# Optimization experiments

Hardware: AMD Instinct MI355X
Metric: run time of the kernel (lower is better)

Reference implementation:

```python
import jax, jax.numpy as jnp
import numpy as np

L, B, D = 1024, 4, 1024
E, K, H = 8, 2, 4096


def setup_inputs() -> dict:
    key = jax.random.key(0)
    ks = jax.random.split(key, 12)
    s_g = 1.0 / np.sqrt(D)
    s_h = 1.0 / np.sqrt(H)
    return {
        "inputs": jax.random.normal(ks[0], (L, B, D), jnp.float32),
        "task_param": jax.random.normal(ks[1], (B, D), jnp.float32),
        "gate_img_w": jax.random.normal(ks[2], (D, E), jnp.float32) * s_g,
        "gate_img_b": jnp.zeros((E,), jnp.float32),
        "gate_txt_w": jax.random.normal(ks[3], (D, E), jnp.float32) * s_g,
        "gate_txt_b": jnp.zeros((E,), jnp.float32),
        "task_gate_w": jax.random.normal(ks[4], (D, E), jnp.float32) * s_g,
        "task_gate_b": jnp.zeros((E,), jnp.float32),
        "alpha": jnp.float32(0.5),
        "w1": jax.random.normal(ks[5], (E, D, H), jnp.float32) * s_g,
        "w2": jax.random.normal(ks[6], (E, H, D), jnp.float32) * s_h,
        "is_text": 1,
    }


def reference(inputs, task_param, gate_img_w, gate_img_b, gate_txt_w, gate_txt_b,
              task_gate_w, task_gate_b, alpha, w1, w2, is_text):
    # task gate: (B, E) -> broadcast over L
    task_logits = (task_param @ task_gate_w + task_gate_b)[None]  # (1, B, E)
    if is_text:
        input_logits = inputs @ gate_txt_w + gate_txt_b  # (L, B, E)
    else:
        input_logits = inputs @ gate_img_w + gate_img_b
    gate_logits = (1.0 - alpha) * input_logits + alpha * task_logits  # (L, B, E)

    topk_vals, sel = jax.lax.top_k(gate_logits, K)  # (L, B, K)

    # auxiliary load-balancing loss
    soft = jax.nn.softmax(gate_logits.astype(jnp.float32), axis=-1)
    avg_weight = soft.mean(axis=(0, 1))                       # (E,)
    expert_mask = jax.nn.one_hot(sel, E).sum(axis=2)          # (L, B, E)
    avg_count = expert_mask.mean(axis=(0, 1))                 # (E,)
    l_aux = jnp.mean(avg_weight * avg_count) * E

    # renormalized top-k weights, combined per expert: (L, B, E)
    weights = jax.nn.softmax(topk_vals.astype(jnp.float32), axis=-1).astype(inputs.dtype)
    comb = jnp.sum(jax.nn.one_hot(sel, E, dtype=weights.dtype) * weights[..., None], axis=2)

    # dense per-expert FFN, weighted combine (loop over fixed small E)
    results = jnp.zeros_like(inputs)
    for e in range(E):
        h = jax.nn.gelu(inputs @ w1[e])      # (L, B, H)
        out = h @ w2[e]                      # (L, B, D)
        results = results + comb[..., e:e + 1] * out
    return results, l_aux.astype(jnp.float32)
```

## Files before the change

kernel.cpp:

```cpp
#include <hip/hip_runtime.h>
#include <hip/hip_bf16.h>
#include <math.h>

#define L_ 1024
#define B_ 4
#define D_ 1024
#define E_ 8
#define K_ 2
#define H_ 4096
#define T_ (L_*B_)
#define P_ (T_*K_)
#define PPAD (P_+256)

typedef unsigned short u16;
typedef __attribute__((ext_vector_type(4))) float f32x4;
typedef __attribute__((ext_vector_type(8))) short s16x8;

__device__ __forceinline__ u16 f2bf(float f) {
  uint32_t u = __float_as_uint(f);
  uint32_t r = (u + 0x7FFFu + ((u >> 16) & 1u)) >> 16;
  return (u16)r;
}
__device__ __forceinline__ float bf2f(u16 v) {
  return __uint_as_float((uint32_t)v << 16);
}
__device__ __forceinline__ float gelu_fast(float v) {
  float u = v * (1.0f + 0.044715f * v * v);
  float t = __expf(-1.5957691216057308f * u);
  return v / (1.0f + t);
}


__device__ void conv_block(const float* __restrict__ src, u16* __restrict__ dst,
                           int R, int C, int r0, int c0) {
  __shared__ float tile[64][65];
  int t = threadIdx.x;
  int tr = t >> 4, tc = (t & 15) * 4;
#pragma unroll
  for (int p = 0; p < 4; ++p) {
    int r = tr + p * 16;
    float4 v = *(const float4*)(src + (size_t)(r0 + r) * C + c0 + tc);
    tile[r][tc] = v.x; tile[r][tc+1] = v.y; tile[r][tc+2] = v.z; tile[r][tc+3] = v.w;
  }
  __syncthreads();
#pragma unroll
  for (int p = 0; p < 4; ++p) {
    int c = tr + p * 16;
    ushort4 o;
    o.x = f2bf(tile[tc+0][c]); o.y = f2bf(tile[tc+1][c]);
    o.z = f2bf(tile[tc+2][c]); o.w = f2bf(tile[tc+3][c]);
    *(ushort4*)(dst + (size_t)(c0 + c) * R + r0 + tc) = o;
  }
}

__global__ void prep(const float* __restrict__ w1, u16* __restrict__ w1b,
                     const float* __restrict__ w2, u16* __restrict__ w2b,
                     const float* __restrict__ x, const float* __restrict__ task_param,
                     const float* __restrict__ gw_img, const float* __restrict__ gb_img,
                     const float* __restrict__ gw_txt, const float* __restrict__ gb_txt,
                     const float* __restrict__ tgw, const float* __restrict__ tgb,
                     const float* __restrict__ alpha_p, const int* __restrict__ is_text_p,
                     float4* __restrict__ sel_w, float* __restrict__ prob_part,
                     int* __restrict__ count_part) {
  int gid = blockIdx.x;
  if (gid < 8192) {
    int gx = gid & 63, gy = (gid >> 6) & 15, e = gid >> 10;
    conv_block(w1 + (size_t)e * D_ * H_, w1b + (size_t)e * D_ * H_,
               D_, H_, gy * 64, gx * 64);
    return;
  }
  if (gid < 16384) {
    int g = gid - 8192;
    int gx = g & 15, gy = (g >> 4) & 63, e = g >> 10;
    conv_block(w2 + (size_t)e * D_ * H_, w2b + (size_t)e * D_ * H_,
               H_, D_, gy * 64, gx * 64);
    return;
  }
  int bid = gid - 16384;
  __shared__ float wprob[4][8];
  __shared__ int wcnt[4][8];
  int wid = threadIdx.x >> 6, lane = threadIdx.x & 63;
  int t = bid * 4 + wid;
  int b = t & (B_ - 1);
  int it = is_text_p[0];
  const float* gw = it ? gw_txt : gw_img;
  const float* gb = it ? gb_txt : gb_img;
  float alpha = alpha_p[0];
  const float* xr = x + (size_t)t * D_;
  const float* tp = task_param + (size_t)b * D_;
  float acc[8] = {0,0,0,0,0,0,0,0};
  float tac[8] = {0,0,0,0,0,0,0,0};
  for (int i = 0; i < D_/64; ++i) {
    int d = i * 64 + lane;
    float xv = xr[d], tv = tp[d];
#pragma unroll
    for (int e = 0; e < 8; ++e) {
      acc[e] += xv * gw[d*8 + e];
      tac[e] += tv * tgw[d*8 + e];
    }
  }
#pragma unroll
  for (int e = 0; e < 8; ++e) {
#pragma unroll
    for (int off = 32; off > 0; off >>= 1) {
      acc[e] += __shfl_xor(acc[e], off);
      tac[e] += __shfl_xor(tac[e], off);
    }
  }
  float lg[8];
#pragma unroll
  for (int e = 0; e < 8; ++e)
    lg[e] = (1.0f - alpha) * (acc[e] + gb[e]) + alpha * (tac[e] + tgb[e]);
  float m = lg[0];
#pragma unroll
  for (int e = 1; e < 8; ++e) m = fmaxf(m, lg[e]);
  float pr[8], ps = 0.f;
#pragma unroll
  for (int e = 0; e < 8; ++e) { pr[e] = expf(lg[e] - m); ps += pr[e]; }
  float inv = 1.0f / ps;
  int i0 = 0; float v0 = lg[0];
#pragma unroll
  for (int e = 1; e < 8; ++e) if (lg[e] > v0) { v0 = lg[e]; i0 = e; }
  int i1 = -1; float v1 = -1e30f;
#pragma unroll
  for (int e = 0; e < 8; ++e) if (e != i0 && lg[e] > v1) { v1 = lg[e]; i1 = e; }
  float ex = expf(v1 - v0);
  float w0 = 1.0f / (1.0f + ex), w1v = ex / (1.0f + ex);
  if (lane == 0) {
    sel_w[t] = make_float4(__int_as_float(i0), __int_as_float(i1), w0, w1v);
#pragma unroll
    for (int e = 0; e < 8; ++e) {
      wprob[wid][e] = pr[e] * inv;
      wcnt[wid][e] = (i0 == e) + (i1 == e);
    }
  }
  __syncthreads();
  if (threadIdx.x < 8) {
    int e = threadIdx.x;
    prob_part[bid * 8 + e] = wprob[0][e] + wprob[1][e] + wprob[2][e] + wprob[3][e];
    count_part[bid * 8 + e] = wcnt[0][e] + wcnt[1][e] + wcnt[2][e] + wcnt[3][e];
  }
}

__global__ void finalize(const float* __restrict__ prob_part, const int* __restrict__ count_part,
                         int* __restrict__ meta, float* __restrict__ laux_out) {
  __shared__ float ps_[256];
  __shared__ int cs_[256];
  int t = threadIdx.x;
  int e = t & 7, s = t >> 3;
  float p = 0.f; int c = 0;
  for (int b = s; b < 1024; b += 32) { p += prob_part[b*8 + e]; c += count_part[b*8 + e]; }
  ps_[t] = p; cs_[t] = c;
  __syncthreads();
  for (int st = 16; st > 0; st >>= 1) {
    if (s < st) { ps_[t] += ps_[t + st*8]; cs_[t] += cs_[t + st*8]; }
    __syncthreads();
  }
  if (t == 0) {
    int off = 0; float laux = 0.f;
    int u1 = 0, u2 = 0;
    for (int ee = 0; ee < 8; ++ee) {
      int cnt = cs_[ee];
      meta[ee] = cnt;
      meta[8 + ee] = off;
      meta[16 + ee] = off;
      int nb = (cnt + 255) >> 8;
      meta[24 + ee] = nb;
      meta[32 + ee] = u1;
      meta[41 + ee] = u2;
      u1 += 16 * nb;
      u2 += 4 * nb * 2;
      off += cnt;
      laux += (ps_[ee] * (1.0f/4096.0f)) * ((float)cnt * (1.0f/4096.0f));
    }
    meta[32 + 8] = u1;
    meta[41 + 8] = u2;
    meta[50] = 0;
    meta[51] = 0;
    *laux_out = laux;
  }
}

__global__ void scatter_gather(const float* __restrict__ x, const float4* __restrict__ sel_w,
                               int* __restrict__ cursors, float* __restrict__ pair_w,
                               int* __restrict__ pair_idx, u16* __restrict__ Xg) {
  int wid = threadIdx.x >> 6, lane = threadIdx.x & 63;
  int t = blockIdx.x * 4 + wid;
  float4 sw = sel_w[t];
  int s0 = __float_as_int(sw.x), s1 = __float_as_int(sw.y);
  int p0 = 0, p1 = 0;
  if (lane == 0) {
    p0 = atomicAdd(&cursors[s0], 1);
    p1 = atomicAdd(&cursors[s1], 1);
  }
  p0 = __shfl(p0, 0); p1 = __shfl(p1, 0);
  if (lane == 0) {
    pair_w[p0] = sw.z; pair_w[p1] = sw.w;
    pair_idx[t*2] = p0; pair_idx[t*2+1] = p1;
  }
  const float* xr = x + (size_t)t * D_;
  u16* d0 = Xg + (size_t)p0 * D_;
  u16* d1 = Xg + (size_t)p1 * D_;
#pragma unroll
  for (int i = 0; i < 4; ++i) {
    int c = i * 256 + lane * 4;
    float4 v = *(const float4*)(xr + c);
    ushort4 o;
    o.x = f2bf(v.x); o.y = f2bf(v.y); o.z = f2bf(v.z); o.w = f2bf(v.w);
    *(ushort4*)(d0 + c) = o;
    *(ushort4*)(d1 + c) = o;
  }
}

template<int EPI, int KDIM, int KLEN, int NOUT, int NPANEL, int KSPLIT>
__global__ __launch_bounds__(512, 2)
void gemm256(const u16* __restrict__ Tok, const u16* __restrict__ Wt,
             int* __restrict__ meta, const float* __restrict__ pair_w,
             u16* __restrict__ Hout, u16* __restrict__ Cout) {
  const int* offs = meta + 8;
  const int* nbx  = meta + 24;
  const int* ub   = (EPI == 0) ? meta + 32 : meta + 41;
  int* tick       = meta + ((EPI == 0) ? 50 : 51);

  __shared__ u16 As[2][16384];
  __shared__ u16 Bs[2][16384];
  __shared__ int s_u;
  int t = threadIdx.x, lane = t & 63, wid = t >> 6;
  int wf = wid & 1, wt = wid >> 1;

  int goff[4]; int ldso[4];
#pragma unroll
  for (int i = 0; i < 4; ++i) {
    int slot = i * 512 + t;
    int row = slot >> 3;
    int kk = (slot & 7) ^ (row & 7);
    goff[i] = row * KDIM + kk * 8;
    ldso[i] = slot * 8;
  }

  int aoff[8][2], boff[4][2];
#pragma unroll
  for (int r = 0; r < 8; ++r) {
    int row = wf * 128 + r * 16 + (lane & 15);
#pragma unroll
    for (int h = 0; h < 2; ++h) {
      int kk = h * 4 + (lane >> 4);
      aoff[r][h] = (row * 8 + (kk ^ (row & 7))) * 8;
    }
  }
#pragma unroll
  for (int f = 0; f < 4; ++f) {
    int row = wt * 64 + f * 16 + (lane & 15);
#pragma unroll
    for (int h = 0; h < 2; ++h) {
      int kk = h * 4 + (lane >> 4);
      boff[f][h] = (row * 8 + (kk ^ (row & 7))) * 8;
    }
  }

  constexpr int NT = KLEN / 64;
  int lr = lane & 15, lg4 = (lane >> 4) * 4;
  int Utot = ub[8];

  for (;;) {
    if (t == 0) s_u = atomicAdd(tick, 1);
    __syncthreads();
    int u = s_u;
    if (u >= Utot) break;
    int e = 0;
    while (u >= ub[e + 1]) ++e;
    int ul = u - ub[e];
    int nb = nbx[e];
    int panel = ul / (nb * KSPLIT);
    int rem   = ul - panel * (nb * KSPLIT);
    int bx    = rem / KSPLIT;
    int ks    = rem - bx * KSPLIT;
    int ne  = meta[e];
    int off = offs[e];
    int kbase = ks * KLEN;
    u16* Cpart = Cout + (size_t)ks * P_ * D_;
    const u16* Wg = Wt + (size_t)e * NOUT * KDIM + (size_t)panel * 256 * KDIM + kbase;
    const u16* Tg = Tok + (size_t)(off + bx * 256) * KDIM + kbase;

    f32x4 acc[8][4] = {};
#pragma unroll
    for (int i = 0; i < 4; ++i) {
      __builtin_amdgcn_global_load_lds(
          (const __attribute__((address_space(1))) void*)(Wg + goff[i]),
          (__attribute__((address_space(3))) void*)(&As[0][ldso[i]]), 16, 0, 0);
      __builtin_amdgcn_global_load_lds(
          (const __attribute__((address_space(1))) void*)(Tg + goff[i]),
          (__attribute__((address_space(3))) void*)(&Bs[0][ldso[i]]), 16, 0, 0);
    }
    __syncthreads();
    int cur = 0;
    for (int tt = 0; tt < NT; ++tt) {
      if (tt + 1 < NT) {
        int k0 = (tt + 1) * 64;
        int nbuf = cur ^ 1;
#pragma unroll
        for (int i = 0; i < 4; ++i) {
          __builtin_amdgcn_global_load_lds(
              (const __attribute__((address_space(1))) void*)(Wg + goff[i] + k0),
              (__attribute__((address_space(3))) void*)(&As[nbuf][ldso[i]]), 16, 0, 0);
          __builtin_amdgcn_global_load_lds(
              (const __attribute__((address_space(1))) void*)(Tg + goff[i] + k0),
              (__attribute__((address_space(3))) void*)(&Bs[nbuf][ldso[i]]), 16, 0, 0);
        }
      }
      const u16* Ab = &As[cur][0]; const u16* Bb = &Bs[cur][0];
#pragma unroll
      for (int h = 0; h < 2; ++h) {
        s16x8 a[8], b[4];
#pragma unroll
        for (int r = 0; r < 8; ++r) a[r] = *(const s16x8*)(Ab + aoff[r][h]);
#pragma unroll
        for (int f = 0; f < 4; ++f) b[f] = *(const s16x8*)(Bb + boff[f][h]);
#pragma unroll
        for (int r = 0; r < 8; ++r)
#pragma unroll
          for (int f = 0; f < 4; ++f)
            acc[r][f] = __builtin_amdgcn_mfma_f32_16x16x32_bf16(a[r], b[f], acc[r][f], 0, 0, 0);
      }
      __syncthreads();
      cur ^= 1;
    }

#pragma unroll
    for (int f = 0; f < 4; ++f) {
      int tokl = bx * 256 + wt * 64 + f * 16 + lr;
      if (tokl >= ne) continue;
      size_t grow = (size_t)(off + tokl);
      if (EPI == 0) {
#pragma unroll
        for (int r = 0; r < 8; ++r) {
          ushort4 o;
          o.x = f2bf(gelu_fast(acc[r][f][0]));
          o.y = f2bf(gelu_fast(acc[r][f][1]));
          o.z = f2bf(gelu_fast(acc[r][f][2]));
          o.w = f2bf(gelu_fast(acc[r][f][3]));
          *(ushort4*)(Hout + grow * NOUT + panel * 256 + wf * 128 + r * 16 + lg4) = o;
        }
      } else {
        float w = pair_w[grow];
#pragma unroll
        for (int r = 0; r < 8; ++r) {
          ushort4 o;
          o.x = f2bf(acc[r][f][0] * w); o.y = f2bf(acc[r][f][1] * w);
          o.z = f2bf(acc[r][f][2] * w); o.w = f2bf(acc[r][f][3] * w);
          *(ushort4*)(Cpart + grow * NOUT + panel * 256 + wf * 128 + r * 16 + lg4) = o;
        }
      }
    }
  }
}

__global__ void combine(const u16* __restrict__ pair_out, const int* __restrict__ pair_idx,
                        float* __restrict__ out) {
  const u16* part1 = pair_out + (size_t)P_ * D_;
  int t = blockIdx.x;
  int p0 = pair_idx[t*2], p1 = pair_idx[t*2+1];
  int c = threadIdx.x * 4;
  ushort4 a0 = *(const ushort4*)(pair_out + (size_t)p0 * D_ + c);
  ushort4 a1 = *(const ushort4*)(part1    + (size_t)p0 * D_ + c);
  ushort4 b0 = *(const ushort4*)(pair_out + (size_t)p1 * D_ + c);
  ushort4 b1 = *(const ushort4*)(part1    + (size_t)p1 * D_ + c);
  float4 o;
  o.x = (bf2f(a0.x) + bf2f(a1.x)) + (bf2f(b0.x) + bf2f(b1.x));
  o.y = (bf2f(a0.y) + bf2f(a1.y)) + (bf2f(b0.y) + bf2f(b1.y));
  o.z = (bf2f(a0.z) + bf2f(a1.z)) + (bf2f(b0.z) + bf2f(b1.z));
  o.w = (bf2f(a0.w) + bf2f(a1.w)) + (bf2f(b0.w) + bf2f(b1.w));
  *(float4*)(out + (size_t)t * D_ + c) = o;
}

extern "C" void kernel_launch(void* const* d_in, const int* in_sizes, int n_in,
                              void* d_out, int out_size, void* d_ws, size_t ws_size,
                              hipStream_t stream) {
  const float* inputs      = (const float*)d_in[0];
  const float* task_param  = (const float*)d_in[1];
  const float* gate_img_w  = (const float*)d_in[2];
  const float* gate_img_b  = (const float*)d_in[3];
  const float* gate_txt_w  = (const float*)d_in[4];
  const float* gate_txt_b  = (const float*)d_in[5];
  const float* task_gate_w = (const float*)d_in[6];
  const float* task_gate_b = (const float*)d_in[7];
  const float* alpha       = (const float*)d_in[8];
  const float* w1          = (const float*)d_in[9];
  const float* w2          = (const float*)d_in[10];
  const int*   is_text     = (const int*)d_in[11];
  float* out = (float*)d_out;

  char* ws = (char*)d_ws;
  u16* w1b = (u16*)(ws + 0);
  u16* w2b = (u16*)(ws + 67108864);
  u16* Xg  = (u16*)(ws + 134217728);
  u16* Hb  = (u16*)(ws + 151519232);
  float4* sel_w   = (float4*)(ws + 220725248);
  float* pair_w   = (float*)(ws + 220725248 + 65536);
  int* pair_idx   = (int*)(ws + 220725248 + 98816);
  float* prob_part= (float*)(ws + 220725248 + 131584);
  int* count_part = (int*)(ws + 220725248 + 164352);
  int* meta       = (int*)(ws + 220725248 + 197120);
  u16* pair_out   = (u16*)(ws + 0);

  prep<<<dim3(17408), 256, 0, stream>>>(w1, w1b, w2, w2b,
      inputs, task_param, gate_img_w, gate_img_b, gate_txt_w, gate_txt_b,
      task_gate_w, task_gate_b, alpha, is_text, sel_w, prob_part, count_part);
  finalize<<<dim3(1), 256, 0, stream>>>(prob_part, count_part, meta,
      out + (size_t)T_ * D_);
  scatter_gather<<<dim3(T_/4), 256, 0, stream>>>(inputs, sel_w, meta + 16, pair_w, pair_idx, Xg);
  gemm256<0, D_, D_, H_, 16, 1><<<dim3(256), 512, 0, stream>>>(
      Xg, w1b, meta, pair_w, Hb, (u16*)nullptr);
  gemm256<1, H_, H_/2, D_, 4, 2><<<dim3(256), 512, 0, stream>>>(
      Hb, w2b, meta, pair_w, (u16*)nullptr, pair_out);
  combine<<<dim3(T_), 256, 0, stream>>>(pair_out, pair_idx, out);
}
```

Measured before the change: 484.1 us.

## Fold w2 bf16 conversion into first GEMM's work queue and split second GEMM K four ways

The w2 fp32-to-bf16 transpose conversion moves out of the prep kernel and becomes extra work units appended to the first expert GEMM's persistent atomic work queue. Those blocks convert w2 tiles after the GEMM tiles are drained, so the memory-bound conversion can overlap with the tail of the compute-bound GEMM. The second GEMM's K split goes from 2 to 4, which raises its unit count, and combine now sums four partial buffers. The cost is more partial-output traffic and bf16 rounding of each partial sum. There is also an ordering risk: the second GEMM depends on the conversion finishing, and only kernel boundaries enforce that.

```diff
diff --git a/kernel.cpp b/kernel.cpp
--- a/kernel.cpp
+++ b/kernel.cpp
@@ -54,7 +54,6 @@
 }
 
 __global__ void prep(const float* __restrict__ w1, u16* __restrict__ w1b,
-                     const float* __restrict__ w2, u16* __restrict__ w2b,
                      const float* __restrict__ x, const float* __restrict__ task_param,
                      const float* __restrict__ gw_img, const float* __restrict__ gb_img,
                      const float* __restrict__ gw_txt, const float* __restrict__ gb_txt,
@@ -69,14 +68,7 @@
                D_, H_, gy * 64, gx * 64);
     return;
   }
-  if (gid < 16384) {
-    int g = gid - 8192;
-    int gx = g & 15, gy = (g >> 4) & 63, e = g >> 10;
-    conv_block(w2 + (size_t)e * D_ * H_, w2b + (size_t)e * D_ * H_,
-               H_, D_, gy * 64, gx * 64);
-    return;
-  }
-  int bid = gid - 16384;
+  int bid = gid - 8192;
   __shared__ float wprob[4][8];
   __shared__ int wcnt[4][8];
   int wid = threadIdx.x >> 6, lane = threadIdx.x & 63;
@@ -169,7 +161,7 @@
       meta[32 + ee] = u1;
       meta[41 + ee] = u2;
       u1 += 16 * nb;
-      u2 += 4 * nb * 2;
+      u2 += 16 * nb;
       off += cnt;
       laux += (ps_[ee] * (1.0f/4096.0f)) * ((float)cnt * (1.0f/4096.0f));
     }
@@ -212,11 +204,12 @@
   }
 }
 
-template<int EPI, int KDIM, int KLEN, int NOUT, int NPANEL, int KSPLIT>
+template<int EPI, int KDIM, int KLEN, int NOUT, int NPANEL, int KSPLIT, bool DOCONV>
 __global__ __launch_bounds__(512, 2)
 void gemm256(const u16* __restrict__ Tok, const u16* __restrict__ Wt,
              int* __restrict__ meta, const float* __restrict__ pair_w,
-             u16* __restrict__ Hout, u16* __restrict__ Cout) {
+             u16* __restrict__ Hout, u16* __restrict__ Cout,
+             const float* __restrict__ w2f, u16* __restrict__ w2b) {
   const int* offs = meta + 8;
   const int* nbx  = meta + 24;
   const int* ub   = (EPI == 0) ? meta + 32 : meta + 41;
@@ -260,13 +253,47 @@
 
   constexpr int NT = KLEN / 64;
   int lr = lane & 15, lg4 = (lane >> 4) * 4;
-  int Utot = ub[8];
+  int Ugemm = ub[8];
+  int Utot = DOCONV ? (Ugemm + 4096) : Ugemm;
 
   for (;;) {
     if (t == 0) s_u = atomicAdd(tick, 1);
     __syncthreads();
     int u = s_u;
     if (u >= Utot) break;
+
+    if (DOCONV && u >= Ugemm) {
+      int cu = u - Ugemm;
+      int e = cu >> 9;
+      int loc = cu & 511;
+      int rb = loc >> 4, cb = loc & 15;
+      int r0 = rb * 128, c0 = cb * 64;
+      const float* src = w2f + (size_t)e * H_ * D_;
+      u16* dst = w2b + (size_t)e * H_ * D_;
+      float* tile = (float*)&As[0][0];
+#pragma unroll
+      for (int p = 0; p < 4; ++p) {
+        int idx = p * 512 + t;
+        int r = idx >> 4;
+        int cq = (idx & 15) * 4;
+        float4 v = *(const float4*)(src + (size_t)(r0 + r) * D_ + c0 + cq);
+        float* tr = tile + r * 67 + cq;
+        tr[0] = v.x; tr[1] = v.y; tr[2] = v.z; tr[3] = v.w;
+      }
+      __syncthreads();
+      int c = t >> 3, rq0 = (t & 7) * 16;
+#pragma unroll
+      for (int j = 0; j < 16; j += 4) {
+        ushort4 o;
+        o.x = f2bf(tile[(rq0 + j + 0) * 67 + c]);
+        o.y = f2bf(tile[(rq0 + j + 1) * 67 + c]);
+        o.z = f2bf(tile[(rq0 + j + 2) * 67 + c]);
+        o.w = f2bf(tile[(rq0 + j + 3) * 67 + c]);
+        *(ushort4*)(dst + (size_t)(c0 + c) * H_ + r0 + rq0 + j) = o;
+      }
+      continue;
+    }
+
     int e = 0;
     while (u >= ub[e + 1]) ++e;
     int ul = u - ub[e];
@@ -357,19 +384,21 @@
 
 __global__ void combine(const u16* __restrict__ pair_out, const int* __restrict__ pair_idx,
                         float* __restrict__ out) {
-  const u16* part1 = pair_out + (size_t)P_ * D_;
   int t = blockIdx.x;
   int p0 = pair_idx[t*2], p1 = pair_idx[t*2+1];
   int c = threadIdx.x * 4;
-  ushort4 a0 = *(const ushort4*)(pair_out + (size_t)p0 * D_ + c);
-  ushort4 a1 = *(const ushort4*)(part1    + (size_t)p0 * D_ + c);
-  ushort4 b0 = *(const ushort4*)(pair_out + (size_t)p1 * D_ + c);
-  ushort4 b1 = *(const ushort4*)(part1    + (size_t)p1 * D_ + c);
-  float4 o;
-  o.x = (bf2f(a0.x) + bf2f(a1.x)) + (bf2f(b0.x) + bf2f(b1.x));
-  o.y = (bf2f(a0.y) + bf2f(a1.y)) + (bf2f(b0.y) + bf2f(b1.y));
-  o.z = (bf2f(a0.z) + bf2f(a1.z)) + (bf2f(b0.z) + bf2f(b1.z));
-  o.w = (bf2f(a0.w) + bf2f(a1.w)) + (bf2f(b0.w) + bf2f(b1.w));
+  float ox = 0.f, oy = 0.f, oz = 0.f, ow = 0.f;
+#pragma unroll
+  for (int part = 0; part < 4; ++part) {
+    const u16* pp = pair_out + (size_t)part * P_ * D_;
+    ushort4 a = *(const ushort4*)(pp + (size_t)p0 * D_ + c);
+    ushort4 b = *(const ushort4*)(pp + (size_t)p1 * D_ + c);
+    ox += bf2f(a.x) + bf2f(b.x);
+    oy += bf2f(a.y) + bf2f(b.y);
+    oz += bf2f(a.z) + bf2f(b.z);
+    ow += bf2f(a.w) + bf2f(b.w);
+  }
+  float4 o; o.x = ox; o.y = oy; o.z = oz; o.w = ow;
   *(float4*)(out + (size_t)t * D_ + c) = o;
 }
 
@@ -403,15 +432,15 @@
   int* meta       = (int*)(ws + 220725248 + 197120);
   u16* pair_out   = (u16*)(ws + 0);
 
-  prep<<<dim3(17408), 256, 0, stream>>>(w1, w1b, w2, w2b,
+  prep<<<dim3(9216), 256, 0, stream>>>(w1, w1b,
       inputs, task_param, gate_img_w, gate_img_b, gate_txt_w, gate_txt_b,
       task_gate_w, task_gate_b, alpha, is_text, sel_w, prob_part, count_part);
   finalize<<<dim3(1), 256, 0, stream>>>(prob_part, count_part, meta,
       out + (size_t)T_ * D_);
   scatter_gather<<<dim3(T_/4), 256, 0, stream>>>(inputs, sel_w, meta + 16, pair_w, pair_idx, Xg);
-  gemm256<0, D_, D_, H_, 16, 1><<<dim3(256), 512, 0, stream>>>(
-      Xg, w1b, meta, pair_w, Hb, (u16*)nullptr);
-  gemm256<1, H_, H_/2, D_, 4, 2><<<dim3(256), 512, 0, stream>>>(
-      Hb, w2b, meta, pair_w, (u16*)nullptr, pair_out);
+  gemm256<0, D_, D_, H_, 16, 1, true><<<dim3(256), 512, 0, stream>>>(
+      Xg, w1b, meta, pair_w, Hb, (u16*)nullptr, w2, w2b);
+  gemm256<1, H_, H_/4, D_, 4, 4, false><<<dim3(256), 512, 0, stream>>>(
+      Hb, w2b, meta, pair_w, (u16*)nullptr, pair_out, (const float*)nullptr, (u16*)nullptr);
   combine<<<dim3(T_), 256, 0, stream>>>(pair_out, pair_idx, out);
 }
```

Result: faster. 450.2 us (median of 2 runs) (-7.0%).
